# Kernel tuning notes

Measured on AMD Instinct MI355X. Metric: run time of the kernel, lower is better.

Reference implementation:

```python
import jax, jax.numpy as jnp
import numpy as np

D_MODEL = 1024
D_STATE = 16
D_CONV = 4
EXPAND = 2
D_INNER = D_MODEL * EXPAND


def setup_inputs() -> dict:
    key = jax.random.key(0)
    ks = jax.random.split(key, 10)
    B, L = 2, 2048
    x = jax.random.normal(ks[0], (B, L, D_MODEL), jnp.float32)
    W_in = jax.random.normal(ks[1], (2 * D_INNER, D_MODEL), jnp.float32) * (1.0 / np.sqrt(D_MODEL))
    conv_w = jax.random.normal(ks[2], (D_INNER, 1, D_CONV), jnp.float32) * (1.0 / np.sqrt(D_CONV))
    conv_b = jax.random.normal(ks[3], (D_INNER,), jnp.float32) * 0.1
    W_x = jax.random.normal(ks[4], (2 * D_STATE + 1, D_INNER), jnp.float32) * (1.0 / np.sqrt(D_INNER))
    A_log = jnp.log(jnp.abs(jax.random.normal(ks[5], (D_INNER, D_STATE), jnp.float32)) + 1e-4)
    D_param = jnp.ones((D_INNER,), jnp.float32)
    W_dt = jax.random.normal(ks[6], (D_INNER, 1), jnp.float32)
    b_dt = jax.random.normal(ks[7], (D_INNER,), jnp.float32) * 0.1
    W_out = jax.random.normal(ks[8], (D_MODEL, D_INNER), jnp.float32) * (1.0 / np.sqrt(D_INNER))
    return {"x": x, "W_in": W_in, "conv_w": conv_w, "conv_b": conv_b, "W_x": W_x,
            "A_log": A_log, "D_param": D_param, "W_dt": W_dt, "b_dt": b_dt, "W_out": W_out}


def _forward(x, W_in, conv_w, conv_b, W_x, A_log, D_param, W_dt, b_dt, W_out):
    B, L, _ = x.shape
    xz = x @ W_in.T                                  # [B,L,2*d_inner]
    x_ssm, z = jnp.split(xz, 2, axis=-1)
    # causal depthwise conv: torch pads both sides d_conv-1 then truncates to L == left-pad only
    xc = jnp.transpose(x_ssm, (0, 2, 1))             # [B,d_inner,L]
    xc = jax.lax.conv_general_dilated(
        xc, conv_w, window_strides=(1,), padding=[(D_CONV - 1, 0)],
        feature_group_count=D_INNER, dimension_numbers=("NCH", "OIH", "NCH"))
    xc = xc + conv_b[None, :, None]
    x_ssm = jax.nn.silu(jnp.transpose(xc, (0, 2, 1)))  # [B,L,d_inner]
    proj = x_ssm @ W_x.T                              # [B,L,2*d_state+1]
    B_ssm = proj[..., :D_STATE]                       # [B,L,d_state]
    C_ssm = proj[..., D_STATE:2 * D_STATE]            # [B,L,d_state]
    dt = jax.nn.softplus(proj[..., -1:] * W_dt[:, 0] + b_dt)  # [B,L,d_inner]
    A = -jnp.exp(A_log)                               # [d_inner,d_state]

    def step(h, inp):
        dt_t, Bt, Ct, xt = inp                        # [B,d_inner],[B,n],[B,n],[B,d_inner]
        dA = jnp.exp(dt_t[..., None] * A)             # [B,d_inner,d_state]
        h = dA * h + (xt * dt_t)[..., None] * Bt[:, None, :]
        y = jnp.einsum("bdn,bn->bd", h, Ct)
        return h, y

    h0 = jnp.zeros((B, D_INNER, D_STATE), x.dtype)
    inputs = (jnp.transpose(dt, (1, 0, 2)), jnp.transpose(B_ssm, (1, 0, 2)),
              jnp.transpose(C_ssm, (1, 0, 2)), jnp.transpose(x_ssm, (1, 0, 2)))
    _, ys = jax.lax.scan(step, h0, inputs)            # ys: [L,B,d_inner]
    y = jnp.transpose(ys, (1, 0, 2)) + x_ssm * D_param
    y = y * jax.nn.silu(z)
    return y @ W_out.T


def reference(x, W_in, conv_w, conv_b, W_x, A_log, D_param, W_dt, b_dt, W_out):
    return _forward(x, W_in, conv_w, conv_b, W_x, A_log, D_param, W_dt, b_dt, W_out)
```

## Files before the change

### kernel.cpp

```cpp
#include <hip/hip_runtime.h>
#include <hip/hip_bf16.h>
#include <cstddef>

#define DMODEL 1024
#define DI     2048
#define DS     16
#define LSEQ   2048
#define BATCH  2
#define NC     128
#define TCH    (LSEQ / NC)

typedef __attribute__((ext_vector_type(8))) short short8;
typedef __attribute__((ext_vector_type(4))) float f32x4;
typedef __attribute__((ext_vector_type(2))) float f32x2;
typedef __attribute__((ext_vector_type(8))) unsigned short us8;

__device__ __forceinline__ unsigned short f2bf(float f) {
    unsigned int u = __float_as_uint(f);
    unsigned int r = (u + 0x7fff + ((u >> 16) & 1)) >> 16;
    return (unsigned short)r;
}
__device__ __forceinline__ float bf2f(unsigned short b) {
    return __uint_as_float(((unsigned int)b) << 16);
}

__device__ __forceinline__ float fexp2(float x) {
#if __has_builtin(__builtin_amdgcn_exp2f)
    return __builtin_amdgcn_exp2f(x);
#else
    return exp2f(x);
#endif
}
__device__ __forceinline__ float flog2(float x) {
#if __has_builtin(__builtin_amdgcn_logf)
    return __builtin_amdgcn_logf(x);
#else
    return log2f(x);
#endif
}

#define LOG2E 1.4426950408889634f
#define RLOG2E 0.6931471805599453f

__device__ __forceinline__ float softplus_f(float v) {
    return (v > 20.f) ? v : flog2(1.f + fexp2(v * LOG2E)) * RLOG2E;
}

__device__ __forceinline__ void gload_lds16(const void* g, void* l) {
    __builtin_amdgcn_global_load_lds(
        (const __attribute__((address_space(1))) unsigned int*)g,
        (__attribute__((address_space(3))) unsigned int*)l, 16, 0, 0);
}

__global__ void cvt_bf16(const float* __restrict__ in, unsigned short* __restrict__ out, int n8) {
    int i = blockIdx.x * 256 + threadIdx.x;
    if (i >= n8) return;
    const float4* p = reinterpret_cast<const float4*>(in) + i * 2;
    float4 v0 = p[0], v1 = p[1];
    us8 o;
    o[0] = f2bf(v0.x); o[1] = f2bf(v0.y); o[2] = f2bf(v0.z); o[3] = f2bf(v0.w);
    o[4] = f2bf(v1.x); o[5] = f2bf(v1.y); o[6] = f2bf(v1.z); o[7] = f2bf(v1.w);
    *reinterpret_cast<us8*>(out + (size_t)i * 8) = o;
}

__global__ void prep_wx(const float* __restrict__ wx, unsigned short* __restrict__ out) {
    int i = blockIdx.x * 256 + threadIdx.x;
    if (i >= 48 * 2048 / 8) return;
    size_t o = (size_t)i * 8;
    int row = (int)(o >> 11);
    us8 v;
    if (row < 33) {
        const float4* p = reinterpret_cast<const float4*>(wx + o);
        float4 v0 = p[0], v1 = p[1];
        v[0] = f2bf(v0.x); v[1] = f2bf(v0.y); v[2] = f2bf(v0.z); v[3] = f2bf(v0.w);
        v[4] = f2bf(v1.x); v[5] = f2bf(v1.y); v[6] = f2bf(v1.z); v[7] = f2bf(v1.w);
    } else {
        v = (us8)0;
    }
    *reinterpret_cast<us8*>(out + o) = v;
}

__global__ void prep_A(const float* __restrict__ A_log, float* __restrict__ At2) {
    int i = blockIdx.x * 256 + threadIdx.x;
    if (i >= DS * DI) return;
    int n = i / DI, d = i % DI;
    At2[i] = -__expf(A_log[d * DS + n]) * LOG2E;
}

#define NT1 32
__global__ __launch_bounds__(512, 2)
void gemm1_pipe(const unsigned short* __restrict__ A, const unsigned short* __restrict__ B,
                unsigned short* __restrict__ C) {
    __shared__ unsigned short lds[4][2][256 * 32];

    const int tid = threadIdx.x;
    const int wid = tid >> 6, ln = tid & 63;
    const int wm = wid >> 2, wn = wid & 3;

    int wg = blockIdx.x;
    wg = (wg & 7) * 32 + (wg >> 3);
    const int m0 = (wg >> 4) * 256;
    const int n0 = (wg & 15) * 256;

    const int srow = tid >> 2;
    const int sun  = tid & 3;
    const int ksrc = ((sun ^ ((srow >> 1) & 3)) * 8);

    const int fr = ln & 15;
    const int fku = (ln >> 4);

    f32x4 acc[8][4] = {};

    #define STAGE1(kt)                                                                     \
        do {                                                                               \
            const int bq_ = (kt) & 3;                                                      \
            gload_lds16(A + (size_t)(m0 + srow) * 1024 + (kt) * 32 + ksrc,                 \
                        &lds[bq_][0][srow * 32 + sun * 8]);                                \
            gload_lds16(A + (size_t)(m0 + 128 + srow) * 1024 + (kt) * 32 + ksrc,           \
                        &lds[bq_][0][(128 + srow) * 32 + sun * 8]);                        \
            gload_lds16(B + (size_t)(n0 + srow) * 1024 + (kt) * 32 + ksrc,                 \
                        &lds[bq_][1][srow * 32 + sun * 8]);                                \
            gload_lds16(B + (size_t)(n0 + 128 + srow) * 1024 + (kt) * 32 + ksrc,           \
                        &lds[bq_][1][(128 + srow) * 32 + sun * 8]);                        \
        } while (0)

    STAGE1(0); STAGE1(1); STAGE1(2);
    asm volatile("s_waitcnt vmcnt(8)" ::: "memory");
    __builtin_amdgcn_s_barrier();
    __builtin_amdgcn_sched_barrier(0);

    for (int kt = 0; kt < NT1; ++kt) {
        const int bq = kt & 3;
        if (kt + 3 < NT1) STAGE1(kt + 3);

        short8 af_lo[4], bfr[4], af_hi[4];
        #pragma unroll
        for (int i = 0; i < 4; ++i) {
            int r = wm * 128 + i * 16 + fr;
            int u = fku ^ ((r >> 1) & 3);
            af_lo[i] = *reinterpret_cast<const short8*>(&lds[bq][0][r * 32 + u * 8]);
        }
        #pragma unroll
        for (int j = 0; j < 4; ++j) {
            int r = wn * 64 + j * 16 + fr;
            int u = fku ^ ((r >> 1) & 3);
            bfr[j] = *reinterpret_cast<const short8*>(&lds[bq][1][r * 32 + u * 8]);
        }
        #pragma unroll
        for (int i = 0; i < 4; ++i) {
            int r = wm * 128 + (4 + i) * 16 + fr;
            int u = fku ^ ((r >> 1) & 3);
            af_hi[i] = *reinterpret_cast<const short8*>(&lds[bq][0][r * 32 + u * 8]);
        }
        __builtin_amdgcn_sched_barrier(0);
        __builtin_amdgcn_s_setprio(1);
        #pragma unroll
        for (int i = 0; i < 4; ++i)
            #pragma unroll
            for (int j = 0; j < 4; ++j)
                acc[i][j] = __builtin_amdgcn_mfma_f32_16x16x32_bf16(af_lo[i], bfr[j], acc[i][j], 0, 0, 0);
        __builtin_amdgcn_s_setprio(0);
        __builtin_amdgcn_sched_barrier(0);
        __builtin_amdgcn_s_setprio(1);
        #pragma unroll
        for (int i = 0; i < 4; ++i)
            #pragma unroll
            for (int j = 0; j < 4; ++j)
                acc[4 + i][j] = __builtin_amdgcn_mfma_f32_16x16x32_bf16(af_hi[i], bfr[j], acc[4 + i][j], 0, 0, 0);
        __builtin_amdgcn_s_setprio(0);
        __builtin_amdgcn_sched_barrier(0);

        if (kt < NT1 - 3)       asm volatile("s_waitcnt vmcnt(8)" ::: "memory");
        else if (kt == NT1 - 3) asm volatile("s_waitcnt vmcnt(4)" ::: "memory");
        else if (kt == NT1 - 2) asm volatile("s_waitcnt vmcnt(0)" ::: "memory");
        __builtin_amdgcn_s_barrier();
        __builtin_amdgcn_sched_barrier(0);
    }
    #undef STAGE1

    const int cr = (ln >> 4) * 4, cc = ln & 15;
    #pragma unroll
    for (int i = 0; i < 8; ++i) {
        int row = m0 + wm * 128 + i * 16 + cr;
        #pragma unroll
        for (int j = 0; j < 4; ++j) {
            int col = n0 + wn * 64 + j * 16 + cc;
            #pragma unroll
            for (int r = 0; r < 4; ++r)
                C[(size_t)(row + r) * 4096 + col] = f2bf(acc[i][j][r]);
        }
    }
}

__global__ __launch_bounds__(256)
void gemm_bf16_nt(const unsigned short* __restrict__ A, int lda,
                  const unsigned short* __restrict__ B, int ldb,
                  float* __restrict__ C, int M, int N, int K) {
    __shared__ unsigned short As[128 * 32];
    __shared__ unsigned short Bs[128 * 32];

    const int tid = threadIdx.x;
    const int wv = tid >> 6, ln = tid & 63;
    const int m0 = blockIdx.y * 128, n0 = blockIdx.x * 128;
    const int wm = wv >> 1, wn = wv & 1;

    f32x4 acc[4][4] = {};

    const int srow = ln >> 2;
    const int scol = (ln & 3) * 8;
    const int fr = ln & 15, fk = (ln >> 4) * 8;

    for (int k0 = 0; k0 < K; k0 += 32) {
        #pragma unroll
        for (int c = 0; c < 2; ++c) {
            int ch = wv * 2 + c;
            gload_lds16(A + (size_t)(m0 + ch * 16 + srow) * lda + k0 + scol, &As[ch * 512]);
            gload_lds16(B + (size_t)(n0 + ch * 16 + srow) * ldb + k0 + scol, &Bs[ch * 512]);
        }
        __syncthreads();

        short8 af[4], bf_[4];
        #pragma unroll
        for (int i = 0; i < 4; ++i) {
            af[i]  = *reinterpret_cast<const short8*>(&As[(wm * 64 + i * 16 + fr) * 32 + fk]);
            bf_[i] = *reinterpret_cast<const short8*>(&Bs[(wn * 64 + i * 16 + fr) * 32 + fk]);
        }
        #pragma unroll
        for (int i = 0; i < 4; ++i)
            #pragma unroll
            for (int j = 0; j < 4; ++j)
                acc[i][j] = __builtin_amdgcn_mfma_f32_16x16x32_bf16(af[i], bf_[j], acc[i][j], 0, 0, 0);
        __syncthreads();
    }

    const int cr = (ln >> 4) * 4, cc = ln & 15;
    #pragma unroll
    for (int i = 0; i < 4; ++i) {
        int row = m0 + wm * 64 + i * 16 + cr;
        #pragma unroll
        for (int j = 0; j < 4; ++j) {
            int col = n0 + wn * 64 + j * 16 + cc;
            #pragma unroll
            for (int r = 0; r < 4; ++r)
                C[(size_t)(row + r) * N + col] = acc[i][j][r];
        }
    }
}

__global__ void conv_silu(const unsigned short* __restrict__ xzb, const float* __restrict__ cw,
                          const float* __restrict__ cb, unsigned short* __restrict__ xactb) {
    int i = blockIdx.x * 256 + threadIdx.x;
    if (i >= BATCH * LSEQ * DI / 8) return;
    int d0 = (i % (DI / 8)) * 8;
    int l  = (i / (DI / 8)) % LSEQ;
    int b  = i / ((DI / 8) * LSEQ);

    float4 w[8];
    #pragma unroll
    for (int j = 0; j < 8; ++j)
        w[j] = *reinterpret_cast<const float4*>(cw + (d0 + j) * 4);

    float acc[8];
    #pragma unroll
    for (int j = 0; j < 8; ++j) acc[j] = cb[d0 + j];

    #pragma unroll
    for (int t = 0; t < 4; ++t) {
        int ls = l - 3 + t;
        if (ls >= 0) {
            us8 v = *reinterpret_cast<const us8*>(xzb + (size_t)(b * LSEQ + ls) * 4096 + d0);
            #pragma unroll
            for (int j = 0; j < 8; ++j) {
                float wt = (t == 0) ? w[j].x : (t == 1) ? w[j].y : (t == 2) ? w[j].z : w[j].w;
                acc[j] += bf2f(v[j]) * wt;
            }
        }
    }
    us8 o;
    #pragma unroll
    for (int j = 0; j < 8; ++j) {
        float v = acc[j] / (1.f + __expf(-acc[j]));
        o[j] = f2bf(v);
    }
    *reinterpret_cast<us8*>(xactb + (size_t)i * 8) = o;
}

__global__ __launch_bounds__(256)
void gemm_proj_mfma(const unsigned short* __restrict__ Xb, const unsigned short* __restrict__ Wxb,
                    float* __restrict__ projp) {
    __shared__ unsigned short As[64 * 32];
    __shared__ unsigned short Bs[48 * 32];

    const int tid = threadIdx.x;
    const int wv = tid >> 6, ln = tid & 63;
    const int m0 = blockIdx.x * 64;
    const int kz = blockIdx.y;
    const int srow = tid >> 2, skoff = (tid & 3) * 8;
    const int fr = ln & 15, fk = (ln >> 4) * 8;

    f32x4 acc[3] = {};

    const int k0base = kz * 512;
    for (int k0 = k0base; k0 < k0base + 512; k0 += 32) {
        gload_lds16(Xb + (size_t)(m0 + srow) * DI + k0 + skoff, &As[wv * 512]);
        if (wv < 3)
            gload_lds16(Wxb + (size_t)srow * DI + k0 + skoff, &Bs[wv * 512]);
        __syncthreads();

        short8 af = *reinterpret_cast<const short8*>(&As[(wv * 16 + fr) * 32 + fk]);
        #pragma unroll
        for (int j = 0; j < 3; ++j) {
            short8 bf_ = *reinterpret_cast<const short8*>(&Bs[(j * 16 + fr) * 32 + fk]);
            acc[j] = __builtin_amdgcn_mfma_f32_16x16x32_bf16(af, bf_, acc[j], 0, 0, 0);
        }
        __syncthreads();
    }

    const int cr = (ln >> 4) * 4, cc = ln & 15;
    #pragma unroll
    for (int j = 0; j < 3; ++j) {
        int col = j * 16 + cc;
        if (col < 33) {
            #pragma unroll
            for (int r = 0; r < 4; ++r) {
                int row = m0 + wv * 16 + cr + r;
                projp[(size_t)row * 144 + kz * 36 + col] = acc[j][r];
            }
        }
    }
}

__global__ void proj_combine(const float* __restrict__ projp, float* __restrict__ proj) {
    int idx = blockIdx.x * 256 + threadIdx.x;
    if (idx >= BATCH * LSEQ * 33) return;
    int row = idx / 33, col = idx % 33;
    float s = 0.f;
    #pragma unroll
    for (int kz = 0; kz < 4; ++kz)
        s += projp[(size_t)row * 144 + kz * 36 + col];
    proj[(size_t)row * 36 + col] = s;
}

__global__ __launch_bounds__(256)
void scan_phase1(const unsigned short* __restrict__ xactb, const float* __restrict__ proj,
                 const float* __restrict__ At2, const float* __restrict__ W_dt,
                 const float* __restrict__ b_dt, unsigned short* __restrict__ Hend,
                 float* __restrict__ dtsum, unsigned short* __restrict__ yloc,
                 unsigned short* __restrict__ XZb) {
    const int d = blockIdx.x * 256 + threadIdx.x;
    const int c = blockIdx.y;
    const int b = blockIdx.z;

    f32x2 A2[DS / 2], h2[DS / 2];
    #pragma unroll
    for (int p = 0; p < DS / 2; ++p) {
        A2[p] = (f32x2){At2[(2 * p) * DI + d], At2[(2 * p + 1) * DI + d]};
        h2[p] = (f32x2){0.f, 0.f};
    }
    const float wdt = W_dt[d], bdt = b_dt[d];
    float ssum = 0.f;

    const int l0 = c * TCH;
    #pragma unroll 2
    for (int l = l0; l < l0 + TCH; ++l) {
        const size_t row = (size_t)(b * LSEQ + l);
        const float* pr = proj + row * 36;
        float dt = softplus_f(pr[32] * wdt + bdt);
        ssum += dt;
        XZb[row * 4096 + d] = f2bf(ssum);
        float x = bf2f(xactb[row * DI + d]);
        float xdt = x * dt;
        f32x2 xdt2 = (f32x2){xdt, xdt};
        f32x2 y2 = (f32x2){0.f, 0.f};
        #pragma unroll
        for (int p = 0; p < DS / 2; ++p) {
            f32x2 t = A2[p] * dt;
            f32x2 e2 = (f32x2){fexp2(t.x), fexp2(t.y)};
            h2[p] = e2 * h2[p] + xdt2 * (f32x2){pr[2 * p], pr[2 * p + 1]};
            y2 += h2[p] * (f32x2){pr[16 + 2 * p], pr[17 + 2 * p]};
        }
        yloc[row * DI + d] = f2bf(y2.x + y2.y);
    }
    size_t base = ((size_t)(b * NC + c) * DS) * DI + d;
    #pragma unroll
    for (int p = 0; p < DS / 2; ++p) {
        Hend[base + (size_t)(2 * p) * DI]     = f2bf(h2[p].x);
        Hend[base + (size_t)(2 * p + 1) * DI] = f2bf(h2[p].y);
    }
    dtsum[(size_t)(b * NC + c) * DI + d] = ssum;
}

__global__ void scan_phase2(unsigned short* __restrict__ H, const float* __restrict__ dtsum,
                            const float* __restrict__ At2) {
    int idx = blockIdx.x * 256 + threadIdx.x;
    int b = idx / (DS * DI);
    int r = idx % (DS * DI);
    int n = r / DI, d = r % DI;
    float A2 = At2[n * DI + d];
    float h = 0.f;
    #pragma unroll 4
    for (int c = 0; c < NC; ++c) {
        size_t off = ((size_t)(b * NC + c) * DS + n) * DI + d;
        float He = bf2f(H[off]);
        float P = fexp2(A2 * dtsum[(size_t)(b * NC + c) * DI + d]);
        H[off] = f2bf(h);
        h = P * h + He;
    }
}

__global__ __launch_bounds__(256)
void scan_phase3(const unsigned short* __restrict__ xactb, const unsigned short* __restrict__ yloc,
                 const float* __restrict__ proj, const float* __restrict__ At2,
                 const float* __restrict__ Dp, const unsigned short* __restrict__ Hin,
                 unsigned short* __restrict__ XZb) {
    const int tid = threadIdx.x;
    const int d = blockIdx.x * 256 + tid;
    const int c = blockIdx.y;
    const int b = blockIdx.z;

    f32x2 A2[DS / 2], Hn2[DS / 2];
    size_t hbase = ((size_t)(b * NC + c) * DS) * DI + d;
    #pragma unroll
    for (int p = 0; p < DS / 2; ++p) {
        A2[p]  = (f32x2){At2[(2 * p) * DI + d], At2[(2 * p + 1) * DI + d]};
        Hn2[p] = (f32x2){bf2f(Hin[hbase + (size_t)(2 * p) * DI]),
                         bf2f(Hin[hbase + (size_t)(2 * p + 1) * DI])};
    }

    const float Dv = Dp[d];
    const int l0 = c * TCH;
    #pragma unroll 2
    for (int l = l0; l < l0 + TCH; ++l) {
        const size_t row = (size_t)(b * LSEQ + l);
        const float* pr = proj + row * 36;
        unsigned short* xzrow = XZb + row * 4096;
        float S  = bf2f(xzrow[d]);
        float yl = bf2f(yloc[row * DI + d]);
        float x  = bf2f(xactb[row * DI + d]);
        float z  = bf2f(xzrow[2048 + d]);
        f32x2 corr2 = (f32x2){0.f, 0.f};
        #pragma unroll
        for (int p = 0; p < DS / 2; ++p) {
            f32x2 t = A2[p] * S;
            f32x2 e2 = (f32x2){fexp2(t.x), fexp2(t.y)};
            corr2 += (f32x2){pr[16 + 2 * p], pr[17 + 2 * p]} * e2 * Hn2[p];
        }
        float y = yl + corr2.x + corr2.y + x * Dv;
        float sz = z / (1.f + __expf(-z));
        xzrow[d] = f2bf(y * sz);
    }
}

extern "C" void kernel_launch(void* const* d_in, const int* in_sizes, int n_in,
                              void* d_out, int out_size, void* d_ws, size_t ws_size,
                              hipStream_t stream) {
    const float* x      = (const float*)d_in[0];
    const float* W_in   = (const float*)d_in[1];
    const float* conv_w = (const float*)d_in[2];
    const float* conv_b = (const float*)d_in[3];
    const float* W_x    = (const float*)d_in[4];
    const float* A_log  = (const float*)d_in[5];
    const float* Dp     = (const float*)d_in[6];
    const float* W_dt   = (const float*)d_in[7];
    const float* b_dt   = (const float*)d_in[8];
    const float* W_out  = (const float*)d_in[9];
    float* out = (float*)d_out;

    char* ws = (char*)d_ws;
    unsigned short* XZb   = (unsigned short*)(ws + 0);
    unsigned short* XACTB = (unsigned short*)(ws + 33554432);
    unsigned short* Xb    = (unsigned short*)(ws + 50331648);
    unsigned short* W_inb = (unsigned short*)(ws + 58720256);
    unsigned short* Hbuf  = (unsigned short*)(ws + 67108864);
    unsigned short* YLOC  = (unsigned short*)(ws + 83886080);
    float* PROJ  = (float*)(ws + 100663296);
    float* DTSUM = (float*)(ws + 101711872);
    float* PROJP = (float*)(ws + 103809024);
    float* Abuf  = (float*)(ws + 106954752);
    unsigned short* W_outb = (unsigned short*)(ws + 108003328);
    unsigned short* Wxb48  = (unsigned short*)(ws + 112197632);

    const int M = BATCH * LSEQ;

    cvt_bf16<<<M * DMODEL / 8 / 256, 256, 0, stream>>>(x, Xb, M * DMODEL / 8);
    cvt_bf16<<<2 * DI * DMODEL / 8 / 256, 256, 0, stream>>>(W_in, W_inb, 2 * DI * DMODEL / 8);
    prep_wx<<<48, 256, 0, stream>>>(W_x, Wxb48);
    prep_A<<<DS * DI / 256, 256, 0, stream>>>(A_log, Abuf);

    gemm1_pipe<<<256, 512, 0, stream>>>(Xb, W_inb, XZb);

    conv_silu<<<BATCH * LSEQ * DI / 8 / 256, 256, 0, stream>>>(XZb, conv_w, conv_b, XACTB);

    gemm_proj_mfma<<<dim3(M / 64, 4), 256, 0, stream>>>(XACTB, Wxb48, PROJP);
    proj_combine<<<(M * 33 + 255) / 256, 256, 0, stream>>>(PROJP, PROJ);

    scan_phase1<<<dim3(DI / 256, NC, BATCH), 256, 0, stream>>>(
        XACTB, PROJ, Abuf, W_dt, b_dt, Hbuf, DTSUM, YLOC, XZb);
    scan_phase2<<<BATCH * DS * DI / 256, 256, 0, stream>>>(Hbuf, DTSUM, Abuf);
    scan_phase3<<<dim3(DI / 256, NC, BATCH), 256, 0, stream>>>(
        XACTB, YLOC, PROJ, Abuf, Dp, Hbuf, XZb);

    cvt_bf16<<<DMODEL * DI / 8 / 256, 256, 0, stream>>>(W_out, W_outb, DMODEL * DI / 8);
    gemm_bf16_nt<<<dim3(DMODEL / 128, M / 128), 256, 0, stream>>>(
        XZb, 4096, W_outb, DI, out, M, DMODEL, DI);
}
```

Measured before the change: 221.7 us.

## Replace output GEMM with 4-stage pipelined, swizzled-LDS 128x64 tile kernel

Replaces the simple double-sync output projection GEMM with a pipelined kernel. It uses a 4-deep LDS ring buffer with explicit vmcnt waits, an XOR-swizzled LDS layout to avoid bank conflicts, and smaller 128x64 tiles so 512 workgroups are launched. Block IDs are remapped for L2 locality, and MFMA sections get raised priority. The input GEMM's launch bounds also drop from 2 to 1 waves-per-EU, which frees registers at the cost of possible occupancy.

```diff
diff --git a/kernel.cpp b/kernel.cpp
--- a/kernel.cpp
+++ b/kernel.cpp
@@ -88,7 +88,7 @@
 }
 
 #define NT1 32
-__global__ __launch_bounds__(512, 2)
+__global__ __launch_bounds__(512, 1)
 void gemm1_pipe(const unsigned short* __restrict__ A, const unsigned short* __restrict__ B,
                 unsigned short* __restrict__ C) {
     __shared__ unsigned short lds[4][2][256 * 32];
@@ -192,57 +192,93 @@
     }
 }
 
-__global__ __launch_bounds__(256)
-void gemm_bf16_nt(const unsigned short* __restrict__ A, int lda,
-                  const unsigned short* __restrict__ B, int ldb,
-                  float* __restrict__ C, int M, int N, int K) {
-    __shared__ unsigned short As[128 * 32];
-    __shared__ unsigned short Bs[128 * 32];
+#define NT3 64
+__global__ __launch_bounds__(256, 2)
+void gemm3_pipe(const unsigned short* __restrict__ A, int lda,
+                const unsigned short* __restrict__ B,
+                float* __restrict__ C) {
+    __shared__ unsigned short As[4][128 * 32];
+    __shared__ unsigned short Bs[4][64 * 32];
 
     const int tid = threadIdx.x;
-    const int wv = tid >> 6, ln = tid & 63;
-    const int m0 = blockIdx.y * 128, n0 = blockIdx.x * 128;
-    const int wm = wv >> 1, wn = wv & 1;
-
-    f32x4 acc[4][4] = {};
-
-    const int srow = ln >> 2;
-    const int scol = (ln & 3) * 8;
-    const int fr = ln & 15, fk = (ln >> 4) * 8;
-
-    for (int k0 = 0; k0 < K; k0 += 32) {
-        #pragma unroll
-        for (int c = 0; c < 2; ++c) {
-            int ch = wv * 2 + c;
-            gload_lds16(A + (size_t)(m0 + ch * 16 + srow) * lda + k0 + scol, &As[ch * 512]);
-            gload_lds16(B + (size_t)(n0 + ch * 16 + srow) * ldb + k0 + scol, &Bs[ch * 512]);
-        }
-        __syncthreads();
-
-        short8 af[4], bf_[4];
+    const int wid = tid >> 6, ln = tid & 63;
+    const int wm = wid >> 1, wn = wid & 1;
+
+    int wg = blockIdx.x;
+    wg = (wg & 7) * 64 + (wg >> 3);
+    const int m0 = (wg >> 4) * 128;
+    const int n0 = (wg & 15) * 64;
+
+    const int srow = tid >> 2;
+    const int sun  = tid & 3;
+    const int ksrc = ((sun ^ ((srow >> 1) & 3)) * 8);
+
+    const int fr = ln & 15;
+    const int fku = (ln >> 4);
+
+    f32x4 acc[4][2] = {};
+
+    #define STAGE3(kt)                                                                     \
+        do {                                                                               \
+            const int bq_ = (kt) & 3;                                                      \
+            gload_lds16(A + (size_t)(m0 + srow) * lda + (kt) * 32 + ksrc,                  \
+                        &As[bq_][srow * 32 + sun * 8]);                                    \
+            gload_lds16(A + (size_t)(m0 + 64 + srow) * lda + (kt) * 32 + ksrc,             \
+                        &As[bq_][(64 + srow) * 32 + sun * 8]);                             \
+            gload_lds16(B + (size_t)(n0 + srow) * 2048 + (kt) * 32 + ksrc,                 \
+                        &Bs[bq_][srow * 32 + sun * 8]);                                    \
+        } while (0)
+
+    STAGE3(0); STAGE3(1); STAGE3(2);
+    asm volatile("s_waitcnt vmcnt(6)" ::: "memory");
+    __builtin_amdgcn_s_barrier();
+    __builtin_amdgcn_sched_barrier(0);
+
+    for (int kt = 0; kt < NT3; ++kt) {
+        const int bq = kt & 3;
+        if (kt + 3 < NT3) STAGE3(kt + 3);
+
+        short8 af[4], bfr[2];
         #pragma unroll
         for (int i = 0; i < 4; ++i) {
-            af[i]  = *reinterpret_cast<const short8*>(&As[(wm * 64 + i * 16 + fr) * 32 + fk]);
-            bf_[i] = *reinterpret_cast<const short8*>(&Bs[(wn * 64 + i * 16 + fr) * 32 + fk]);
-        }
+            int r = wm * 64 + i * 16 + fr;
+            int u = fku ^ ((r >> 1) & 3);
+            af[i] = *reinterpret_cast<const short8*>(&As[bq][r * 32 + u * 8]);
+        }
+        #pragma unroll
+        for (int j = 0; j < 2; ++j) {
+            int r = wn * 32 + j * 16 + fr;
+            int u = fku ^ ((r >> 1) & 3);
+            bfr[j] = *reinterpret_cast<const short8*>(&Bs[bq][r * 32 + u * 8]);
+        }
+        __builtin_amdgcn_sched_barrier(0);
+        __builtin_amdgcn_s_setprio(1);
         #pragma unroll
         for (int i = 0; i < 4; ++i)
             #pragma unroll
-            for (int j = 0; j < 4; ++j)
-                acc[i][j] = __builtin_amdgcn_mfma_f32_16x16x32_bf16(af[i], bf_[j], acc[i][j], 0, 0, 0);
-        __syncthreads();
-    }
+            for (int j = 0; j < 2; ++j)
+                acc[i][j] = __builtin_amdgcn_mfma_f32_16x16x32_bf16(af[i], bfr[j], acc[i][j], 0, 0, 0);
+        __builtin_amdgcn_s_setprio(0);
+        __builtin_amdgcn_sched_barrier(0);
+
+        if (kt < NT3 - 3)       asm volatile("s_waitcnt vmcnt(6)" ::: "memory");
+        else if (kt == NT3 - 3) asm volatile("s_waitcnt vmcnt(3)" ::: "memory");
+        else if (kt == NT3 - 2) asm volatile("s_waitcnt vmcnt(0)" ::: "memory");
+        __builtin_amdgcn_s_barrier();
+        __builtin_amdgcn_sched_barrier(0);
+    }
+    #undef STAGE3
 
     const int cr = (ln >> 4) * 4, cc = ln & 15;
     #pragma unroll
     for (int i = 0; i < 4; ++i) {
         int row = m0 + wm * 64 + i * 16 + cr;
         #pragma unroll
-        for (int j = 0; j < 4; ++j) {
-            int col = n0 + wn * 64 + j * 16 + cc;
+        for (int j = 0; j < 2; ++j) {
+            int col = n0 + wn * 32 + j * 16 + cc;
             #pragma unroll
             for (int r = 0; r < 4; ++r)
-                C[(size_t)(row + r) * N + col] = acc[i][j][r];
+                C[(size_t)(row + r) * 1024 + col] = acc[i][j][r];
         }
     }
 }
@@ -501,6 +537,5 @@
         XACTB, YLOC, PROJ, Abuf, Dp, Hbuf, XZb);
 
     cvt_bf16<<<DMODEL * DI / 8 / 256, 256, 0, stream>>>(W_out, W_outb, DMODEL * DI / 8);
-    gemm_bf16_nt<<<dim3(DMODEL / 128, M / 128), 256, 0, stream>>>(
-        XZb, 4096, W_outb, DI, out, M, DMODEL, DI);
-}
+    gemm3_pipe<<<512, 256, 0, stream>>>(XZb, 4096, W_outb, out);
+}
```

After: 211.5 us. -4.6%, faster.
